# Performance work log

Hardware: AMD Instinct MI355X
Metric: run time of the kernel (lower is better)

## Reference

```python
import jax, jax.numpy as jnp
import numpy as np

N_NODES = 50000
N_EDGES = 600000
DIM = 128  # dim == num_kernels (required by the original forward's double filter application)


def setup_inputs() -> dict:
    key = jax.random.key(0)
    ks = jax.random.split(key, 10)
    s = 1.0 / np.sqrt(DIM)
    return {
        "x": jax.random.normal(ks[0], (N_NODES, DIM), dtype=jnp.float32),
        "i": jax.random.randint(ks[1], (N_EDGES,), 0, N_NODES),
        "j": jax.random.randint(ks[2], (N_EDGES,), 0, N_NODES),
        "rbf": jax.random.uniform(ks[3], (N_EDGES, DIM), dtype=jnp.float32),
        "Wl": jax.random.normal(ks[4], (DIM, DIM), dtype=jnp.float32) * s,
        "bl": jnp.zeros((DIM,), dtype=jnp.float32),
        "W0": jax.random.normal(ks[5], (DIM, DIM), dtype=jnp.float32) * s,
        "b0": jnp.zeros((DIM,), dtype=jnp.float32),
        "W2": jax.random.normal(ks[6], (DIM, DIM), dtype=jnp.float32) * s,
        "b2": jnp.zeros((DIM,), dtype=jnp.float32),
        "gamma": jnp.ones((DIM,), dtype=jnp.float32),
        "beta": jnp.zeros((DIM,), dtype=jnp.float32),
    }


def reference(x, i, j, rbf, Wl, bl, W0, b0, W2, b2, gamma, beta):
    # Wxh = lin(x)
    Wxh = x @ Wl.T + bl  # [N, D]
    # m = rbf @ filter[0].weight.T  (no bias), then full filter Sequential on m
    m = rbf @ W0.T                                   # [E, D]
    m = jax.nn.silu(m @ W0.T + b0) @ W2.T + b2       # filter(m): Lin0 -> SiLU -> Lin2
    # scatter-add messages m * Wxh[j] into destination nodes i
    msg = m * Wxh[j]                                 # [E, D] gather + multiply
    agg = jax.ops.segment_sum(msg, i, num_segments=x.shape[0])  # [N, D]
    # residual + LayerNorm
    h = x + agg
    mu = jnp.mean(h, axis=-1, keepdims=True)
    var = jnp.mean(jnp.square(h - mu), axis=-1, keepdims=True)
    return (h - mu) / jnp.sqrt(var + 1e-5) * gamma + beta
```

## Files before the change

### kernel.cpp

```cpp
#include <hip/hip_runtime.h>
#include <math.h>

#define D 128

typedef __attribute__((ext_vector_type(8))) short short8_t;
typedef __attribute__((ext_vector_type(4))) float f32x4;
typedef __attribute__((ext_vector_type(2))) float f32x2;

__device__ __forceinline__ short f2bf(float f) {
  union { float f; unsigned u; } v; v.f = f;
  unsigned r = v.u + 0x7FFFu + ((v.u >> 16) & 1u);
  return (short)(r >> 16);
}
__device__ __forceinline__ float bf2f(unsigned u16) {
  union { unsigned u; float f; } v; v.u = u16 << 16; return v.f;
}

__global__ void prep_kernel(const float* __restrict__ W0, const float* __restrict__ W2,
                            const float* __restrict__ Wl,
                            short* __restrict__ Wcb, short* __restrict__ W2b,
                            short* __restrict__ Wlb, int* __restrict__ count,
                            float* __restrict__ h, int N, int nb, long h4) {
  int b = blockIdx.x, t = threadIdx.x;
  if (b < 64) {
    int idx = b * 256 + t;
    int r = idx >> 7, c = idx & 127;
    float s = 0.f;
    for (int k = 0; k < D; ++k) s += W0[r * D + k] * W0[k * D + c];
    Wcb[idx] = f2bf(s);
  } else if (b < 128) {
    int idx = (b - 64) * 256 + t;
    W2b[idx] = f2bf(W2[idx]);
  } else if (b < 192) {
    int idx = (b - 128) * 256 + t;
    Wlb[idx] = f2bf(Wl[idx]);
  } else if (b < 192 + nb) {
    int idx = (b - 192) * 256 + t;
    if (idx < N) count[idx] = 0;
  } else {
    long i = (long)(b - 192 - nb) * 256 + t;
    long stride = (long)(gridDim.x - 192 - nb) * 256;
    f32x4 z = {0.f, 0.f, 0.f, 0.f};
    for (; i < h4; i += stride) ((f32x4*)h)[i] = z;
  }
}

__global__ void hist_kernel(const int* __restrict__ gi, int* __restrict__ count, int E) {
  int t = blockIdx.x * 256 + threadIdx.x;
  int base = t * 4;
  if (base + 3 < E) {
    int4 v = *(const int4*)(gi + base);
    atomicAdd(&count[v.x], 1);
    atomicAdd(&count[v.y], 1);
    atomicAdd(&count[v.z], 1);
    atomicAdd(&count[v.w], 1);
  } else {
    for (int k = base; k < E; ++k) atomicAdd(&count[gi[k]], 1);
  }
}

__global__ __launch_bounds__(256) void scan_a_kernel(const int* __restrict__ count,
                                                     int* __restrict__ pref,
                                                     int* __restrict__ bsum, int N) {
  __shared__ int ws[4];
  const int tid = threadIdx.x, lane = tid & 63, wave = tid >> 6;
  int i = blockIdx.x * 256 + tid;
  int c = (i < N) ? count[i] : 0;
  int v = c;
#pragma unroll
  for (int o = 1; o < 64; o <<= 1) {
    int u = __shfl_up(v, o, 64);
    if (lane >= o) v += u;
  }
  if (lane == 63) ws[wave] = v;
  __syncthreads();
  int wp = 0;
  for (int w = 0; w < wave; ++w) wp += ws[w];
  if (i < N) pref[i] = wp + v - c;
  if (tid == 255) bsum[blockIdx.x] = wp + v;
}

__global__ __launch_bounds__(256) void scan_c_kernel(const int* __restrict__ pref,
                                                     const int* __restrict__ bsum,
                                                     int* __restrict__ woff, int N) {
  __shared__ int base_s;
  const int tid = threadIdx.x, lane = tid & 63;
  if (tid < 64) {
    int p = 0;
    for (int k = lane; k < blockIdx.x; k += 64) p += bsum[k];
#pragma unroll
    for (int o = 32; o; o >>= 1) p += __shfl_xor(p, o, 64);
    if (lane == 0) base_s = p;
  }
  __syncthreads();
  int i = blockIdx.x * 256 + tid;
  if (i < N) woff[i] = pref[i] + base_s;
}

__global__ void scatter_kernel(const int* __restrict__ gi, const int* __restrict__ gj,
                               int* __restrict__ woff, int4* __restrict__ edata, int E) {
  int e = blockIdx.x * 256 + threadIdx.x;
  if (e < E) {
    int i = gi[e];
    int pos = atomicAdd(&woff[i], 1);
    int4 ed; ed.x = e; ed.y = gj[e]; ed.z = i; ed.w = 0;
    edata[pos] = ed;
  }
}

__global__ __launch_bounds__(256, 2) void node_gemm_kernel(
    const float* __restrict__ x, const short* __restrict__ Wlb,
    const float* __restrict__ bl, short* __restrict__ WxhB, int N) {
  __shared__ short Wl_s[D * D];
  const int tid = threadIdx.x;
  const int lane = tid & 63, wave = tid >> 6;
  const int q = lane & 15, g = lane >> 4;

  for (int it = 0; it < 8; ++it) {
    int eoff = (it * 256 + tid) * 8;
    int row = eoff >> 7, col = eoff & 127;
    int scol = col ^ ((row & 7) << 3);
    *(short8_t*)&Wl_s[row * D + scol] = *(const short8_t*)&Wlb[eoff];
  }

  const int rbase = blockIdx.x * 64 + wave * 16;
  int arow = rbase + q; if (arow > N - 1) arow = N - 1;
  short8_t a[4];
  const float* src = x + (size_t)arow * D;
#pragma unroll
  for (int c = 0; c < 4; ++c) {
    int kb = c * 32 + g * 8;
    f32x4 v0 = *(const f32x4*)(src + kb);
    f32x4 v1 = *(const f32x4*)(src + kb + 4);
    short8_t t;
    t[0]=f2bf(v0.x); t[1]=f2bf(v0.y); t[2]=f2bf(v0.z); t[3]=f2bf(v0.w);
    t[4]=f2bf(v1.x); t[5]=f2bf(v1.y); t[6]=f2bf(v1.z); t[7]=f2bf(v1.w);
    a[c] = t;
  }

  __syncthreads();

  f32x4 acc[8];
#pragma unroll
  for (int n = 0; n < 8; ++n) acc[n] = f32x4{0.f, 0.f, 0.f, 0.f};
#pragma unroll
  for (int n = 0; n < 8; ++n) {
    int row = n * 16 + q;
    int sw = (row & 7) << 3;
#pragma unroll
    for (int c = 0; c < 4; ++c) {
      int col = (c * 32 + g * 8) ^ sw;
      short8_t b = *(const short8_t*)&Wl_s[row * D + col];
      acc[n] = __builtin_amdgcn_mfma_f32_16x16x32_bf16(a[c], b, acc[n], 0, 0, 0);
    }
  }

#pragma unroll
  for (int n = 0; n < 8; ++n) {
    int col = n * 16 + q;
    float bias = bl[col];
#pragma unroll
    for (int r = 0; r < 4; ++r) {
      int orow = rbase + g * 4 + r;
      if (orow < N) WxhB[(size_t)orow * D + col] = f2bf(acc[n][r] + bias);
    }
  }
}

__global__ __launch_bounds__(256, 2) void fused_edge_kernel(
    const float* __restrict__ rbf, const float* __restrict__ b0v,
    const float* __restrict__ b2v, const short* __restrict__ Wcb,
    const short* __restrict__ W2b, const short* __restrict__ WxhB,
    const int4* __restrict__ edata, float* __restrict__ h, int E, int ntiles) {
  __shared__ short Wc_s[D * D];
  __shared__ short W2_s[D * D];
  __shared__ short m_s[4][16 * D];

  const int tid = threadIdx.x;
  const int lane = tid & 63, wave = tid >> 6;
  const int q = lane & 15, g = lane >> 4;

  for (int it = 0; it < 8; ++it) {
    int eoff = (it * 256 + tid) * 8;
    int row = eoff >> 7, col = eoff & 127;
    int scol = col ^ ((row & 7) << 3);
    *(short8_t*)&Wc_s[row * D + scol] = *(const short8_t*)&Wcb[eoff];
    *(short8_t*)&W2_s[row * D + scol] = *(const short8_t*)&W2b[eoff];
  }

  float b0r[8], b2r[8];
#pragma unroll
  for (int n = 0; n < 8; ++n) { b0r[n] = b0v[n * 16 + q]; b2r[n] = b2v[n * 16 + q]; }

  __syncthreads();

  short* ms = &m_s[wave][0];
  const int stride = gridDim.x;

  int tile = blockIdx.x;
  if (tile >= ntiles) return;

#define EQOF(t) ({ int tc_ = (t) < ntiles ? (t) : ntiles - 1;                  \
                   int e_ = tc_ * 64 + wave * 16 + q;                          \
                   e_ < E ? e_ : E - 1; })

  int4 ed0 = edata[EQOF(tile)];
  int4 ed1 = edata[EQOF(tile + stride)];
  int4 ed2 = edata[EQOF(tile + 2 * stride)];
  f32x4 rb[8];
  {
    const float* src = rbf + (size_t)ed0.x * D;
#pragma unroll
    for (int c = 0; c < 4; ++c) {
      rb[c * 2]     = *(const f32x4*)(src + c * 32 + g * 8);
      rb[c * 2 + 1] = *(const f32x4*)(src + c * 32 + g * 8 + 4);
    }
  }
  unsigned wv0[16];
#pragma unroll
  for (int r = 0; r < 16; ++r) {
    int jr = __shfl(ed0.y, r, 64);
    wv0[r] = *(const unsigned*)&WxhB[(size_t)jr * D + lane * 2];
  }

  while (true) {
    const bool hnext = (tile + stride) < ntiles;

    short8_t a[4];
#pragma unroll
    for (int c = 0; c < 4; ++c) {
      f32x4 v0 = rb[c * 2], v1 = rb[c * 2 + 1];
      short8_t t;
      t[0]=f2bf(v0.x); t[1]=f2bf(v0.y); t[2]=f2bf(v0.z); t[3]=f2bf(v0.w);
      t[4]=f2bf(v1.x); t[5]=f2bf(v1.y); t[6]=f2bf(v1.z); t[7]=f2bf(v1.w);
      a[c] = t;
    }

    int4 ed3 = edata[EQOF(tile + 3 * stride)];
    {
      const float* src = rbf + (size_t)ed1.x * D;
#pragma unroll
      for (int c = 0; c < 4; ++c) {
        rb[c * 2]     = *(const f32x4*)(src + c * 32 + g * 8);
        rb[c * 2 + 1] = *(const f32x4*)(src + c * 32 + g * 8 + 4);
      }
    }
    unsigned wv1[16];
#pragma unroll
    for (int r = 0; r < 16; ++r) {
      int jr = __shfl(ed1.y, r, 64);
      wv1[r] = *(const unsigned*)&WxhB[(size_t)jr * D + lane * 2];
    }

    f32x4 acc[8];
#pragma unroll
    for (int n = 0; n < 8; ++n) acc[n] = f32x4{0.f, 0.f, 0.f, 0.f};
#pragma unroll
    for (int n = 0; n < 8; ++n) {
      int row = n * 16 + q;
      int sw = (row & 7) << 3;
#pragma unroll
      for (int c = 0; c < 4; ++c) {
        int col = (c * 32 + g * 8) ^ sw;
        short8_t b = *(const short8_t*)&Wc_s[row * D + col];
        acc[n] = __builtin_amdgcn_mfma_f32_16x16x32_bf16(a[c], b, acc[n], 0, 0, 0);
      }
    }

#pragma unroll
    for (int n = 0; n < 8; ++n) {
      int col = n * 16 + q;
#pragma unroll
      for (int r = 0; r < 4; ++r) {
        int row = g * 4 + r;
        float u = acc[n][r] + b0r[n];
        float s = u / (1.0f + __expf(-u));
        ms[row * D + (col ^ ((row & 7) << 3))] = f2bf(s);
      }
    }

    short8_t a2[4];
    {
      int sw = (q & 7) << 3;
#pragma unroll
      for (int c = 0; c < 4; ++c) {
        int col = (c * 32 + g * 8) ^ sw;
        a2[c] = *(const short8_t*)&ms[q * D + col];
      }
    }

#pragma unroll
    for (int n = 0; n < 8; ++n) acc[n] = f32x4{0.f, 0.f, 0.f, 0.f};
#pragma unroll
    for (int n = 0; n < 8; ++n) {
      int row = n * 16 + q;
      int sw = (row & 7) << 3;
#pragma unroll
      for (int c = 0; c < 4; ++c) {
        int col = (c * 32 + g * 8) ^ sw;
        short8_t b = *(const short8_t*)&W2_s[row * D + col];
        acc[n] = __builtin_amdgcn_mfma_f32_16x16x32_bf16(a2[c], b, acc[n], 0, 0, 0);
      }
    }

#pragma unroll
    for (int n = 0; n < 8; ++n) {
      int col = n * 16 + q;
#pragma unroll
      for (int r = 0; r < 4; ++r) {
        int row = g * 4 + r;
        ms[row * D + (col ^ ((row & 7) << 3))] = f2bf(acc[n][r] + b2r[n]);
      }
    }

    const int eb = tile * 64 + wave * 16;
    int nv = E - eb; if (nv > 16) nv = 16;
    float a0 = 0.f, a1 = 0.f;
    int cur = -1;
#pragma unroll
    for (int r = 0; r < 16; ++r) {
      if (r < nv) {
        int ir = __shfl(ed0.z, r, 64);
        if (ir != cur) {
          if (cur >= 0) {
            float* dst = &h[(size_t)cur * D + lane * 2];
            __hip_atomic_fetch_add(dst, a0, __ATOMIC_RELAXED, __HIP_MEMORY_SCOPE_AGENT);
            __hip_atomic_fetch_add(dst + 1, a1, __ATOMIC_RELAXED, __HIP_MEMORY_SCOPE_AGENT);
            a0 = a1 = 0.f;
          }
          cur = ir;
        }
        unsigned mv = *(const unsigned*)&ms[r * D + ((lane * 2) ^ ((r & 7) << 3))];
        a0 += bf2f(mv & 0xffffu) * bf2f(wv0[r] & 0xffffu);
        a1 += bf2f(mv >> 16) * bf2f(wv0[r] >> 16);
      }
    }
    if (cur >= 0) {
      float* dst = &h[(size_t)cur * D + lane * 2];
      __hip_atomic_fetch_add(dst, a0, __ATOMIC_RELAXED, __HIP_MEMORY_SCOPE_AGENT);
      __hip_atomic_fetch_add(dst + 1, a1, __ATOMIC_RELAXED, __HIP_MEMORY_SCOPE_AGENT);
    }

    if (!hnext) break;
    tile += stride;
    ed0 = ed1; ed1 = ed2; ed2 = ed3;
#pragma unroll
    for (int r = 0; r < 16; ++r) wv0[r] = wv1[r];
  }
#undef EQOF
}

__global__ __launch_bounds__(256) void ln_kernel(const float* __restrict__ agg,
                                                 const float* __restrict__ x,
                                                 const float* __restrict__ gamma,
                                                 const float* __restrict__ beta,
                                                 float* __restrict__ out, int N) {
  int wave = threadIdx.x >> 6, lane = threadIdx.x & 63;
  long row = (long)blockIdx.x * 4 + wave;
  if (row >= N) return;
  int c = lane * 2;
  f32x2 av = *(const f32x2*)&agg[row * D + c];
  f32x2 xv = *(const f32x2*)&x[row * D + c];
  float h0 = av.x + xv.x, h1 = av.y + xv.y;
  float sum = h0 + h1;
  float sq = h0 * h0 + h1 * h1;
#pragma unroll
  for (int o = 32; o; o >>= 1) {
    sum += __shfl_xor(sum, o, 64);
    sq += __shfl_xor(sq, o, 64);
  }
  float mu = sum * (1.0f / 128.0f);
  float var = sq * (1.0f / 128.0f) - mu * mu;
  float rstd = rsqrtf(var + 1e-5f);
  f32x2 gv = *(const f32x2*)&gamma[c];
  f32x2 bv = *(const f32x2*)&beta[c];
  f32x2 ov;
  ov.x = (h0 - mu) * rstd * gv.x + bv.x;
  ov.y = (h1 - mu) * rstd * gv.y + bv.y;
  *(f32x2*)&out[row * D + c] = ov;
}

extern "C" void kernel_launch(void* const* d_in, const int* in_sizes, int n_in,
                              void* d_out, int out_size, void* d_ws, size_t ws_size,
                              hipStream_t stream) {
  const float* x    = (const float*)d_in[0];
  const int*   gi   = (const int*)d_in[1];
  const int*   gj   = (const int*)d_in[2];
  const float* rbf  = (const float*)d_in[3];
  const float* Wl   = (const float*)d_in[4];
  const float* bl   = (const float*)d_in[5];
  const float* W0   = (const float*)d_in[6];
  const float* b0   = (const float*)d_in[7];
  const float* W2   = (const float*)d_in[8];
  const float* b2   = (const float*)d_in[9];
  const float* gam  = (const float*)d_in[10];
  const float* bet  = (const float*)d_in[11];

  const int N = in_sizes[0] / D;
  const int E = in_sizes[1];

  char* ws = (char*)d_ws;
  size_t off = 0;
  float* h    = (float*)(ws + off); off += (size_t)N * D * 4;
  short* WxhB = (short*)(ws + off); off += (size_t)N * D * 2;
  int4*  edat = (int4*)(ws + off);  off += (size_t)E * 16;
  int*   cnt  = (int*)(ws + off);   off += (size_t)N * 4;
  int*   pref = (int*)(ws + off);   off += (size_t)N * 4;
  int*   woff = (int*)(ws + off);   off += (size_t)N * 4;
  int*   bsum = (int*)(ws + off);   off += 1024;
  short* Wcb  = (short*)(ws + off); off += D * D * 2;
  short* W2b  = (short*)(ws + off); off += D * D * 2;
  short* Wlb  = (short*)(ws + off); off += D * D * 2;

  const int ntiles = (E + 63) / 64;
  const int nb = (N + 255) / 256;

  prep_kernel<<<192 + nb + 1024, 256, 0, stream>>>(W0, W2, Wl, Wcb, W2b, Wlb,
                                                   cnt, h, N, nb, (long)N * D / 4);
  hist_kernel<<<(E / 4 + 255) / 256, 256, 0, stream>>>(gi, cnt, E);
  scan_a_kernel<<<nb, 256, 0, stream>>>(cnt, pref, bsum, N);
  scan_c_kernel<<<nb, 256, 0, stream>>>(pref, bsum, woff, N);
  scatter_kernel<<<(E + 255) / 256, 256, 0, stream>>>(gi, gj, woff, edat, E);
  node_gemm_kernel<<<(N + 63) / 64, 256, 0, stream>>>(x, Wlb, bl, WxhB, N);
  fused_edge_kernel<<<512, 256, 0, stream>>>(rbf, b0, b2, Wcb, W2b, WxhB,
                                             edat, h, E, ntiles);
  ln_kernel<<<(N + 3) / 4, 256, 0, stream>>>(h, x, gam, bet, (float*)d_out, N);
}
```

Measured before the change: 254.5 us.

## Fuse gather-multiply-scatter directly on MFMA accumulator layout, skip LDS staging

```diff
diff --git a/kernel.cpp b/kernel.cpp
--- a/kernel.cpp
+++ b/kernel.cpp
@@ -216,15 +216,19 @@
       rb[c * 2 + 1] = *(const f32x4*)(src + c * 32 + g * 8 + 4);
     }
   }
-  unsigned wv0[16];
-#pragma unroll
-  for (int r = 0; r < 16; ++r) {
-    int jr = __shfl(ed0.y, r, 64);
-    wv0[r] = *(const unsigned*)&WxhB[(size_t)jr * D + lane * 2];
-  }
 
   while (true) {
     const bool hnext = (tile + stride) < ntiles;
+    const int eb = tile * 64 + wave * 16;
+
+    int jr[4], ir[4];
+    bool val[4];
+#pragma unroll
+    for (int rr = 0; rr < 4; ++rr) {
+      jr[rr] = __shfl(ed0.y, g * 4 + rr, 64);
+      ir[rr] = __shfl(ed0.z, g * 4 + rr, 64);
+      val[rr] = (eb + g * 4 + rr) < E;
+    }
 
     short8_t a[4];
 #pragma unroll
@@ -245,11 +249,14 @@
         rb[c * 2 + 1] = *(const f32x4*)(src + c * 32 + g * 8 + 4);
       }
     }
-    unsigned wv1[16];
-#pragma unroll
-    for (int r = 0; r < 16; ++r) {
-      int jr = __shfl(ed1.y, r, 64);
-      wv1[r] = *(const unsigned*)&WxhB[(size_t)jr * D + lane * 2];
+
+    unsigned short wv[4][8];
+#pragma unroll
+    for (int rr = 0; rr < 4; ++rr) {
+      const short* wrow = WxhB + (size_t)jr[rr] * D + q;
+#pragma unroll
+      for (int n = 0; n < 8; ++n)
+        wv[rr][n] = *(const unsigned short*)(wrow + n * 16);
     }
 
     f32x4 acc[8];
@@ -303,49 +310,41 @@
       }
     }
 
-#pragma unroll
-    for (int n = 0; n < 8; ++n) {
-      int col = n * 16 + q;
-#pragma unroll
-      for (int r = 0; r < 4; ++r) {
-        int row = g * 4 + r;
-        ms[row * D + (col ^ ((row & 7) << 3))] = f2bf(acc[n][r] + b2r[n]);
-      }
-    }
-
-    const int eb = tile * 64 + wave * 16;
-    int nv = E - eb; if (nv > 16) nv = 16;
-    float a0 = 0.f, a1 = 0.f;
+    float sum[8];
+#pragma unroll
+    for (int n = 0; n < 8; ++n) sum[n] = 0.f;
     int cur = -1;
 #pragma unroll
-    for (int r = 0; r < 16; ++r) {
-      if (r < nv) {
-        int ir = __shfl(ed0.z, r, 64);
-        if (ir != cur) {
+    for (int rr = 0; rr < 4; ++rr) {
+      if (val[rr]) {
+        if (ir[rr] != cur) {
           if (cur >= 0) {
-            float* dst = &h[(size_t)cur * D + lane * 2];
-            __hip_atomic_fetch_add(dst, a0, __ATOMIC_RELAXED, __HIP_MEMORY_SCOPE_AGENT);
-            __hip_atomic_fetch_add(dst + 1, a1, __ATOMIC_RELAXED, __HIP_MEMORY_SCOPE_AGENT);
-            a0 = a1 = 0.f;
+            float* dst = &h[(size_t)cur * D + q];
+#pragma unroll
+            for (int n = 0; n < 8; ++n) {
+              __hip_atomic_fetch_add(dst + n * 16, sum[n],
+                                     __ATOMIC_RELAXED, __HIP_MEMORY_SCOPE_AGENT);
+              sum[n] = 0.f;
+            }
           }
-          cur = ir;
+          cur = ir[rr];
         }
-        unsigned mv = *(const unsigned*)&ms[r * D + ((lane * 2) ^ ((r & 7) << 3))];
-        a0 += bf2f(mv & 0xffffu) * bf2f(wv0[r] & 0xffffu);
-        a1 += bf2f(mv >> 16) * bf2f(wv0[r] >> 16);
+#pragma unroll
+        for (int n = 0; n < 8; ++n)
+          sum[n] += (acc[n][rr] + b2r[n]) * bf2f(wv[rr][n]);
       }
     }
     if (cur >= 0) {
-      float* dst = &h[(size_t)cur * D + lane * 2];
-      __hip_atomic_fetch_add(dst, a0, __ATOMIC_RELAXED, __HIP_MEMORY_SCOPE_AGENT);
-      __hip_atomic_fetch_add(dst + 1, a1, __ATOMIC_RELAXED, __HIP_MEMORY_SCOPE_AGENT);
+      float* dst = &h[(size_t)cur * D + q];
+#pragma unroll
+      for (int n = 0; n < 8; ++n)
+        __hip_atomic_fetch_add(dst + n * 16, sum[n],
+                               __ATOMIC_RELAXED, __HIP_MEMORY_SCOPE_AGENT);
     }
 
     if (!hnext) break;
     tile += stride;
     ed0 = ed1; ed1 = ed2; ed2 = ed3;
-#pragma unroll
-    for (int r = 0; r < 16; ++r) wv0[r] = wv1[r];
   }
 #undef EQOF
 }
```

New measurement: 408.4 us. 1.61x slower.

## Keep composed filter weights in registers and convert Wl inside node GEMM

Applied to the files above, without the earlier changes.

```diff
diff --git a/kernel.cpp b/kernel.cpp
--- a/kernel.cpp
+++ b/kernel.cpp
@@ -17,10 +17,9 @@
 }
 
 __global__ void prep_kernel(const float* __restrict__ W0, const float* __restrict__ W2,
-                            const float* __restrict__ Wl,
                             short* __restrict__ Wcb, short* __restrict__ W2b,
-                            short* __restrict__ Wlb, int* __restrict__ count,
-                            float* __restrict__ h, int N, int nb, long h4) {
+                            int* __restrict__ count, float* __restrict__ h,
+                            int N, int nb, long h4) {
   int b = blockIdx.x, t = threadIdx.x;
   if (b < 64) {
     int idx = b * 256 + t;
@@ -31,15 +30,12 @@
   } else if (b < 128) {
     int idx = (b - 64) * 256 + t;
     W2b[idx] = f2bf(W2[idx]);
-  } else if (b < 192) {
+  } else if (b < 128 + nb) {
     int idx = (b - 128) * 256 + t;
-    Wlb[idx] = f2bf(Wl[idx]);
-  } else if (b < 192 + nb) {
-    int idx = (b - 192) * 256 + t;
     if (idx < N) count[idx] = 0;
   } else {
-    long i = (long)(b - 192 - nb) * 256 + t;
-    long stride = (long)(gridDim.x - 192 - nb) * 256;
+    long i = (long)(b - 128 - nb) * 256 + t;
+    long stride = (long)(gridDim.x - 128 - nb) * 256;
     f32x4 z = {0.f, 0.f, 0.f, 0.f};
     for (; i < h4; i += stride) ((f32x4*)h)[i] = z;
   }
@@ -109,7 +105,7 @@
 }
 
 __global__ __launch_bounds__(256, 2) void node_gemm_kernel(
-    const float* __restrict__ x, const short* __restrict__ Wlb,
+    const float* __restrict__ x, const float* __restrict__ Wl,
     const float* __restrict__ bl, short* __restrict__ WxhB, int N) {
   __shared__ short Wl_s[D * D];
   const int tid = threadIdx.x;
@@ -120,7 +116,12 @@
     int eoff = (it * 256 + tid) * 8;
     int row = eoff >> 7, col = eoff & 127;
     int scol = col ^ ((row & 7) << 3);
-    *(short8_t*)&Wl_s[row * D + scol] = *(const short8_t*)&Wlb[eoff];
+    f32x4 v0 = *(const f32x4*)&Wl[eoff];
+    f32x4 v1 = *(const f32x4*)&Wl[eoff + 4];
+    short8_t t;
+    t[0]=f2bf(v0.x); t[1]=f2bf(v0.y); t[2]=f2bf(v0.z); t[3]=f2bf(v0.w);
+    t[4]=f2bf(v1.x); t[5]=f2bf(v1.y); t[6]=f2bf(v1.z); t[7]=f2bf(v1.w);
+    *(short8_t*)&Wl_s[row * D + scol] = t;
   }
 
   const int rbase = blockIdx.x * 64 + wave * 16;
@@ -172,7 +173,6 @@
     const float* __restrict__ b2v, const short* __restrict__ Wcb,
     const short* __restrict__ W2b, const short* __restrict__ WxhB,
     const int4* __restrict__ edata, float* __restrict__ h, int E, int ntiles) {
-  __shared__ short Wc_s[D * D];
   __shared__ short W2_s[D * D];
   __shared__ short m_s[4][16 * D];
 
@@ -184,8 +184,16 @@
     int eoff = (it * 256 + tid) * 8;
     int row = eoff >> 7, col = eoff & 127;
     int scol = col ^ ((row & 7) << 3);
-    *(short8_t*)&Wc_s[row * D + scol] = *(const short8_t*)&Wcb[eoff];
     *(short8_t*)&W2_s[row * D + scol] = *(const short8_t*)&W2b[eoff];
+  }
+
+  short8_t wcf[8][4];
+#pragma unroll
+  for (int n = 0; n < 8; ++n) {
+    const short* wrow = Wcb + (n * 16 + q) * D + g * 8;
+#pragma unroll
+    for (int c = 0; c < 4; ++c)
+      wcf[n][c] = *(const short8_t*)(wrow + c * 32);
   }
 
   float b0r[8], b2r[8];
@@ -256,16 +264,10 @@
 #pragma unroll
     for (int n = 0; n < 8; ++n) acc[n] = f32x4{0.f, 0.f, 0.f, 0.f};
 #pragma unroll
-    for (int n = 0; n < 8; ++n) {
-      int row = n * 16 + q;
-      int sw = (row & 7) << 3;
-#pragma unroll
-      for (int c = 0; c < 4; ++c) {
-        int col = (c * 32 + g * 8) ^ sw;
-        short8_t b = *(const short8_t*)&Wc_s[row * D + col];
-        acc[n] = __builtin_amdgcn_mfma_f32_16x16x32_bf16(a[c], b, acc[n], 0, 0, 0);
-      }
-    }
+    for (int n = 0; n < 8; ++n)
+#pragma unroll
+      for (int c = 0; c < 4; ++c)
+        acc[n] = __builtin_amdgcn_mfma_f32_16x16x32_bf16(a[c], wcf[n][c], acc[n], 0, 0, 0);
 
 #pragma unroll
     for (int n = 0; n < 8; ++n) {
@@ -410,18 +412,17 @@
   int*   bsum = (int*)(ws + off);   off += 1024;
   short* Wcb  = (short*)(ws + off); off += D * D * 2;
   short* W2b  = (short*)(ws + off); off += D * D * 2;
-  short* Wlb  = (short*)(ws + off); off += D * D * 2;
 
   const int ntiles = (E + 63) / 64;
   const int nb = (N + 255) / 256;
 
-  prep_kernel<<<192 + nb + 1024, 256, 0, stream>>>(W0, W2, Wl, Wcb, W2b, Wlb,
+  prep_kernel<<<128 + nb + 1024, 256, 0, stream>>>(W0, W2, Wcb, W2b,
                                                    cnt, h, N, nb, (long)N * D / 4);
   hist_kernel<<<(E / 4 + 255) / 256, 256, 0, stream>>>(gi, cnt, E);
   scan_a_kernel<<<nb, 256, 0, stream>>>(cnt, pref, bsum, N);
   scan_c_kernel<<<nb, 256, 0, stream>>>(pref, bsum, woff, N);
   scatter_kernel<<<(E + 255) / 256, 256, 0, stream>>>(gi, gj, woff, edat, E);
-  node_gemm_kernel<<<(N + 63) / 64, 256, 0, stream>>>(x, Wlb, bl, WxhB, N);
+  node_gemm_kernel<<<(N + 63) / 64, 256, 0, stream>>>(x, Wl, bl, WxhB, N);
   fused_edge_kernel<<<512, 256, 0, stream>>>(rbf, b0, b2, Wcb, W2b, WxhB,
                                              edat, h, E, ntiles);
   ln_kernel<<<(N + 3) / 4, 256, 0, stream>>>(h, x, gam, bet, (float*)d_out, N);
```

After: 314.8 us. 23.7% more time.
